# Performance work log

Measured on AMD Instinct MI355X. Metric: run time of the kernel, lower is better.

The kernel has to match this reference:

```python
import jax, jax.numpy as jnp
import numpy as np
from jax import lax

B, L, C, P = 512, 6, 4, 45

def _conv(x, w, b, pad):
    y = lax.conv_general_dilated(x, w, (1, 1), [(pad, pad), (pad, pad)],
                                 dimension_numbers=('NCHW', 'OIHW', 'NCHW'))
    return y + b[None, :, None, None]

def _maxpool2(x):
    return lax.reduce_window(x, -jnp.inf, lax.max, (1, 1, 2, 2), (1, 1, 2, 2), 'VALID')

def _prelu(x, a):
    return jnp.where(x >= 0, x, a * x)

def setup_inputs() -> dict:
    key = jax.random.key(0)
    ks = jax.random.split(key, 16)
    s = 0.05
    inp = {
        'x': jax.random.normal(ks[0], (B, L, C, P, P), jnp.float32),
        'w0': jax.random.normal(ks[1], (32, C, 5, 5), jnp.float32) * s,
        'b0': jnp.zeros((32,), jnp.float32),
        'w1': jax.random.normal(ks[2], (32, 32, 5, 5), jnp.float32) * s,
        'b1': jnp.zeros((32,), jnp.float32),
        'w2': jax.random.normal(ks[3], (64, 32, 4, 4), jnp.float32) * s,
        'b2': jnp.zeros((64,), jnp.float32),
        'w3': jax.random.normal(ks[4], (64, 64, 3, 3), jnp.float32) * s,
        'b3': jnp.zeros((64,), jnp.float32),
        'a0': jnp.float32(0.25), 'a1': jnp.float32(0.25),
        'a2': jnp.float32(0.25), 'a3': jnp.float32(0.25),
        'fc1_w': jax.random.normal(ks[5], (L, 256, 128), jnp.float32) * s,
        'fc1_b': jnp.zeros((L, 128), jnp.float32),
        'a4': jnp.full((L, 1), 0.25, jnp.float32),
        'fc2_w': jax.random.normal(ks[6], (L, 128, 64), jnp.float32) * s,
        'fc2_b': jnp.zeros((L, 64), jnp.float32),
        'a5': jnp.full((L, 1), 0.25, jnp.float32),
        'fc3_w': jax.random.normal(ks[7], (L, 64, 4), jnp.float32) * s,
        'fc3_b': jnp.zeros((L, 4), jnp.float32),
    }
    return inp

def reference(x, w0, b0, w1, b1, w2, b2, w3, b3, a0, a1, a2, a3,
              fc1_w, fc1_b, a4, fc2_w, fc2_b, a5, fc3_w, fc3_b):
    b, l = x.shape[0], x.shape[1]
    # Conv tower shares weights across landmarks -> fold landmark into batch.
    h = x.reshape(b * l, x.shape[2], P, P)
    h = _maxpool2(_prelu(_conv(h, w0, b0, 1), a0))   # (BL,32,21,21)
    h = _maxpool2(_prelu(_conv(h, w1, b1, 1), a1))   # (BL,32,9,9)
    h = _maxpool2(_prelu(_conv(h, w2, b2, 1), a2))   # (BL,64,4,4)
    h = _prelu(_conv(h, w3, b3, 0), a3)              # (BL,64,2,2)
    h = h.reshape(b, l, 256)
    # Per-landmark FC heads as batched GEMMs.
    h = _prelu(jnp.einsum('bli,lio->blo', h, fc1_w) + fc1_b, a4)
    h = _prelu(jnp.einsum('bli,lio->blo', h, fc2_w) + fc2_b, a5)
    out = jnp.einsum('bli,lio->blo', h, fc3_w) + fc3_b   # (B,L,4)
    return out
```

## Files before the change

### kernel.cpp

```cpp
#include <hip/hip_runtime.h>
#include <stdint.h>

typedef _Float16 f16;
typedef _Float16 half8 __attribute__((ext_vector_type(8)));
typedef _Float16 half4 __attribute__((ext_vector_type(4)));
typedef float floatx16 __attribute__((ext_vector_type(16)));

#define NIMG 3072

#define WS_W0T   0
#define WS_W1T   10240
#define WS_W2T   61440
#define WS_W3T   126976
#define WS_FC1T  200704
#define WS_FC2T  593920
#define WS_FC3T  692224
#define WS_H3F   16646144

#define Z16 {0.f,0.f,0.f,0.f,0.f,0.f,0.f,0.f,0.f,0.f,0.f,0.f,0.f,0.f,0.f,0.f}

#define TOF(t) ((((t) > 24 ? 24 : (t)) / 5) * 208 + (((t) > 24 ? 24 : (t)) % 5) * 4)

__global__ __launch_bounds__(256) void k_prep(
    const float* __restrict__ w0, const float* __restrict__ w1, const float* __restrict__ w2,
    const float* __restrict__ w3, const float* __restrict__ fc1w, const float* __restrict__ fc2w,
    const float* __restrict__ fc3w,
    f16* __restrict__ w0t, f16* __restrict__ w1t, f16* __restrict__ w2t, f16* __restrict__ w3t,
    f16* __restrict__ fc1t, f16* __restrict__ fc2t, f16* __restrict__ fc3t)
{
  int stride = gridDim.x * blockDim.x;
  int g0 = blockIdx.x * blockDim.x + threadIdx.x;
  for (int i = g0; i < 3584; i += stride) {
    int j = i & 7, co = (i >> 3) & 31, hf = (i >> 8) & 1, t = i >> 9;
    int k = t * 16 + hf * 8 + j, tap = k >> 2, ci = k & 3;
    f16 v = (f16)0.f;
    if (tap < 25) { int ky = tap / 5, kx = tap % 5; v = (f16)w0[((co * 4 + ci) * 5 + ky) * 5 + kx]; }
    w0t[i] = v;
  }
  for (int i = g0; i < 25600; i += stride) {
    int j = i & 7, co = (i >> 3) & 31, hf = (i >> 8) & 1, ch = (i >> 9) & 1, tap = i >> 10;
    int ci = ch * 16 + hf * 8 + j, ky = tap / 5, kx = tap % 5;
    w1t[i] = (f16)w1[((co * 32 + ci) * 5 + ky) * 5 + kx];
  }
  for (int i = g0; i < 32768; i += stride) {
    int j = i & 7, co = (i >> 3) & 31, hf = (i >> 8) & 1, ct = (i >> 9) & 1, ch = (i >> 10) & 1, tap = i >> 11;
    int ci = ch * 16 + hf * 8 + j, cog = ct * 32 + co, ky = tap >> 2, kx = tap & 3;
    w2t[i] = (f16)w2[((cog * 32 + ci) * 4 + ky) * 4 + kx];
  }
  for (int i = g0; i < 36864; i += stride) {
    int j = i & 7, col = (i >> 3) & 31, hf = (i >> 8) & 1, ct = (i >> 9) & 1, c = i >> 10;
    int k = c * 16 + hf * 8 + j, tap = k >> 6, ci = k & 63, co = ct * 32 + col;
    int ky = tap / 3, kx = tap % 3;
    w3t[i] = (f16)w3[((co * 64 + ci) * 3 + ky) * 3 + kx];
  }
  for (int i = g0; i < 196608; i += stride) {
    int j = i & 7, col = (i >> 3) & 31, hf = (i >> 8) & 1, nt = (i >> 9) & 3, c = (i >> 11) & 15, l = i >> 15;
    int k = c * 16 + hf * 8 + j, o = nt * 32 + col;
    fc1t[i] = (f16)fc1w[(l * 256 + k) * 128 + o];
  }
  for (int i = g0; i < 49152; i += stride) {
    int j = i & 7, col = (i >> 3) & 31, hf = (i >> 8) & 1, nt = (i >> 9) & 1, c = (i >> 10) & 7, l = i >> 13;
    int k = c * 16 + hf * 8 + j, o = nt * 32 + col;
    fc2t[i] = (f16)fc2w[(l * 128 + k) * 64 + o];
  }
  for (int i = g0; i < 12288; i += stride) {
    int j = i & 7, col = (i >> 3) & 31, hf = (i >> 8) & 1, c = (i >> 9) & 3, l = i >> 11;
    int k = c * 16 + hf * 8 + j;
    f16 v = (f16)0.f;
    if (col < 4) v = (f16)fc3w[(l * 64 + k) * 4 + col];
    fc3t[i] = v;
  }
}

__global__ __launch_bounds__(512, 6) void k_conv012(
    const float* __restrict__ x,
    const f16* __restrict__ w0t, const float* __restrict__ b0, const float* __restrict__ a0p,
    const f16* __restrict__ w1t, const float* __restrict__ b1, const float* __restrict__ a1p,
    const f16* __restrict__ w2t, const float* __restrict__ b2, const float* __restrict__ a2p,
    f16* __restrict__ h3f)
{
  __shared__ __align__(16) uint32_t smem_u[12688];
  f16* sh   = (f16*)smem_u;
  f16* s_h1 = sh;
  f16* s_x  = sh + 22880;

  const int n = blockIdx.x, tid = threadIdx.x;
  const int wv = tid >> 6, l = tid & 63;
  const int hf = l >> 5, m = l & 31, dr = m >> 3, dc = m & 7, col = m;
  const float a0 = a0p[0], a1 = a1p[0];
  const float b0c = b0[col], b1c = b1[col];
  const half8* w0t8 = (const half8*)w0t;
  const half8* w1t8 = (const half8*)w1t;
  const half8* w2t8 = (const half8*)w2t;

  for (int i = tid; i < 2096; i += 512) {
    int cell = i >> 4, wi = i & 15, r, c;
    if (cell < 26) { r = 0; c = cell; }
    else { int j = cell - 26; r = j / 5 + 1; int c5 = j % 5; c = (c5 == 0) ? 0 : 21 + c5; }
    smem_u[(r * 26 + c) * 20 + wi] = 0u;
  }

  half8 B0[7];
  #pragma unroll
  for (int q = 0; q < 7; ++q)
    B0[q] = w0t8[(q * 2 + hf) * 32 + col];

  const int cdr = (m & 1) | ((m & 8) >> 2);
  const int cdc = ((m >> 1) & 3) | ((m & 16) >> 2);
  const float* xin = x + n * 8100;

  for (int band = 0; band < 6; ++band) {
    const int lo    = (band < 5) ? band * 8 : 38;
    const int nrows = (band < 5) ? 12 : 8;
    const int tend  = (band < 5) ? band * 12 + 12 : 66;
    for (int i = tid; i < nrows * 52; i += 512) {
      int rp = lo + i / 52, cp = i % 52;
      half4 h = {(f16)0, (f16)0, (f16)0, (f16)0};
      if (rp >= 1 && rp <= 45 && cp >= 1 && cp <= 45) {
        const float* px = xin + (rp - 1) * 45 + (cp - 1);
        h[0] = (f16)px[0];
        h[1] = (f16)px[2025];
        h[2] = (f16)px[4050];
        h[3] = (f16)px[6075];
      }
      *(half4*)(s_x + ((rp - lo) * 52 + cp) * 4) = h;
    }
    __syncthreads();
    for (int t = band * 12 + wv; t < tend; t += 8) {
      int g = t / 6;
      int r0 = 4 * g; if (r0 > 38) r0 = 38;
      int cb = (t % 6) * 8;
      int rowb = r0 - lo + cdr, colb = cb + cdc;
      const f16* base = s_x + (rowb * 52 + colb) * 4;
      floatx16 acc = Z16;
      #pragma unroll
      for (int q = 0; q < 7; ++q) {
        const int offL = hf ? TOF(4 * q + 2) : TOF(4 * q);
        half4 lo4 = *(const half4*)(base + offL);
        half4 hi4;
        if (q < 6) {
          const int offH = hf ? TOF(4 * q + 3) : TOF(4 * q + 1);
          hi4 = *(const half4*)(base + offH);
        } else {
          hi4 = (half4){(f16)0, (f16)0, (f16)0, (f16)0};
        }
        half8 av = __builtin_shufflevector(lo4, hi4, 0, 1, 2, 3, 4, 5, 6, 7);
        acc = __builtin_amdgcn_mfma_f32_32x32x16_f16(av, B0[q], acc, 0, 0, 0);
      }
      #pragma unroll
      for (int q = 0; q < 4; ++q) {
        float v = fmaxf(fmaxf(acc[4*q], acc[4*q + 1]), fmaxf(acc[4*q + 2], acc[4*q + 3]));
        v += b0c; v = (v >= 0.f) ? v : a0 * v;
        int pr = (r0 >> 1) + (q & 1), pc = (cb >> 1) + hf + 2 * (q >> 1);
        if (pc < 21) s_h1[((pr + 1) * 26 + (pc + 1)) * 40 + col] = (f16)v;
      }
    }
    __syncthreads();
  }

  int t0 = wv * 2;
  int t1 = t0 + 1; if (t1 > 14) t1 = 14;
  int r0a = 4 * (t0 / 3); if (r0a > 14) r0a = 14;
  int cca = 8 * (t0 % 3); if (cca > 14) cca = 14;
  int r0b = 4 * (t1 / 3); if (r0b > 14) r0b = 14;
  int ccb = 8 * (t1 % 3); if (ccb > 14) ccb = 14;
  const f16* pAa = s_h1 + ((r0a + dr) * 26 + cca + dc) * 40 + hf * 8;
  const f16* pAb = s_h1 + ((r0b + dr) * 26 + ccb + dc) * 40 + hf * 8;
  floatx16 accA = Z16;
  floatx16 accB = Z16;
  for (int ky = 0; ky < 5; ++ky) {
    const half8* wb = w1t8 + ky * 640 + hf * 32 + col;
    const f16* qa = pAa + ky * 1040;
    const f16* qb = pAb + ky * 1040;
    #pragma unroll
    for (int kx = 0; kx < 5; ++kx) {
      #pragma unroll
      for (int ch = 0; ch < 2; ++ch) {
        half8 b  = wb[kx * 128 + ch * 64];
        half8 aA = *(const half8*)(qa + kx * 40 + ch * 16);
        half8 aB = *(const half8*)(qb + kx * 40 + ch * 16);
        accA = __builtin_amdgcn_mfma_f32_32x32x16_f16(aA, b, accA, 0, 0, 0);
        accB = __builtin_amdgcn_mfma_f32_32x32x16_f16(aB, b, accB, 0, 0, 0);
      }
    }
  }
  __syncthreads();

  f16* s2 = sh;
  for (int i = tid; i < 640; i += 512) {
    int cell = i >> 4, wi = i & 15, r, c;
    if (cell < 11)      { r = 0;  c = cell; }
    else if (cell < 22) { r = 10; c = cell - 11; }
    else if (cell < 31) { r = cell - 21; c = 0; }
    else                { r = cell - 30; c = 10; }
    smem_u[(r * 14 + c) * 20 + wi] = 0u;
  }
  #pragma unroll
  for (int tt = 0; tt < 2; ++tt) {
    const floatx16 acc = tt ? accB : accA;
    int r0 = tt ? r0b : r0a, cc = tt ? ccb : cca;
    #pragma unroll
    for (int pp = 0; pp < 2; ++pp)
      #pragma unroll
      for (int c2 = 0; c2 < 2; ++c2) {
        float v = fmaxf(fmaxf(acc[8*pp + 2*c2], acc[8*pp + 2*c2 + 1]),
                        fmaxf(acc[8*pp + 4 + 2*c2], acc[8*pp + 4 + 2*c2 + 1]));
        v += b1c; v = (v >= 0.f) ? v : a1 * v;
        int pr = (r0 >> 1) + pp, pc = (cc >> 1) + 2 * hf + c2;
        if (pc < 9) s2[((pr + 1) * 14 + (pc + 1)) * 40 + col] = (f16)v;
      }
  }
  __syncthreads();

  if (wv < 4) {
    const int mt = wv >> 1, c2t = wv & 1;
    const float a2 = a2p[0];
    const float b2c = b2[c2t * 32 + col];
    const f16* pA = s2 + ((mt * 4 + dr) * 14 + dc) * 40 + hf * 8;
    floatx16 acc = Z16;
    #pragma unroll 4
    for (int tap = 0; tap < 16; ++tap) {
      int aoff = ((tap >> 2) * 14 + (tap & 3)) * 40;
      #pragma unroll
      for (int ch = 0; ch < 2; ++ch) {
        half8 b = w2t8[tap * 256 + ch * 128 + c2t * 64 + hf * 32 + col];
        half8 a = *(const half8*)(pA + aoff + ch * 16);
        acc = __builtin_amdgcn_mfma_f32_32x32x16_f16(a, b, acc, 0, 0, 0);
      }
    }
    f16* o = h3f + n * 1024;
    #pragma unroll
    for (int pp = 0; pp < 2; ++pp)
      #pragma unroll
      for (int c2 = 0; c2 < 2; ++c2) {
        float v = fmaxf(fmaxf(acc[8*pp + 2*c2], acc[8*pp + 2*c2 + 1]),
                        fmaxf(acc[8*pp + 4 + 2*c2], acc[8*pp + 4 + 2*c2 + 1]));
        v += b2c; v = (v >= 0.f) ? v : a2 * v;
        int pr = mt * 2 + pp, pc = 2 * hf + c2;
        o[(pr * 4 + pc) * 64 + c2t * 32 + col] = (f16)v;
      }
  }
}

__global__ __launch_bounds__(256) void k_tail(
    const f16* __restrict__ h3f,
    const f16* __restrict__ w3t, const float* __restrict__ b3, const float* __restrict__ a3p,
    const f16* __restrict__ fc1t, const float* __restrict__ fc1b, const float* __restrict__ a4,
    const f16* __restrict__ fc2t, const float* __restrict__ fc2b, const float* __restrict__ a5,
    const f16* __restrict__ fc3t, const float* __restrict__ fc3b,
    float* __restrict__ out)
{
  __shared__ __align__(16) f16 s_feat[32 * 264];
  __shared__ __align__(16) f16 s_g1[32 * 136];
  __shared__ __align__(16) f16 s_g2[32 * 72];

  const int lm = blockIdx.x % 6, t = blockIdx.x / 6;
  const int tid = threadIdx.x, wv = tid >> 6, lane = tid & 63;
  const int hf = lane >> 5, col = lane & 31;
  const half8* w3t8  = (const half8*)w3t;
  const half8* fc1t8 = (const half8*)fc1t;
  const half8* fc2t8 = (const half8*)fc2t;
  const half8* fc3t8 = (const half8*)fc3t;

  {
    const int mt = wv;
    const int i_img = mt * 8 + (col >> 2);
    const int pos = col & 3, oy = pos >> 1, ox = pos & 1;
    const int gimg = (t * 32 + i_img) * 6 + lm;
    const f16* Abase = h3f + gimg * 1024 + (oy * 4 + ox) * 64;
    floatx16 acc0 = Z16, acc1 = Z16;
    for (int c = 0; c < 36; ++c) {
      int tap = c >> 2;
      int ky = tap / 3, kx = tap % 3;
      half8 a = *(const half8*)(Abase + (ky * 4 + kx) * 64 + (c & 3) * 16 + hf * 8);
      half8 bb0 = w3t8[((c * 2 + 0) * 2 + hf) * 32 + col];
      half8 bb1 = w3t8[((c * 2 + 1) * 2 + hf) * 32 + col];
      acc0 = __builtin_amdgcn_mfma_f32_32x32x16_f16(a, bb0, acc0, 0, 0, 0);
      acc1 = __builtin_amdgcn_mfma_f32_32x32x16_f16(a, bb1, acc1, 0, 0, 0);
    }
    const float a3 = a3p[0];
    #pragma unroll
    for (int ct = 0; ct < 2; ++ct) {
      const floatx16 acc = ct ? acc1 : acc0;
      const int co = ct * 32 + col;
      const float bb = b3[co];
      #pragma unroll
      for (int q = 0; q < 4; ++q) {
        int ii = mt * 8 + 2 * q + hf;
        half4 w;
        #pragma unroll
        for (int z = 0; z < 4; ++z) {
          float v = acc[q * 4 + z] + bb;
          v = (v >= 0.f) ? v : a3 * v;
          w[z] = (f16)v;
        }
        *(half4*)(s_feat + ii * 264 + co * 4) = w;
      }
    }
  }
  __syncthreads();

  {
    floatx16 g = Z16;
    for (int c = 0; c < 16; ++c) {
      half8 a = *(const half8*)(s_feat + col * 264 + c * 16 + hf * 8);
      half8 b = fc1t8[(((lm * 16 + c) * 4 + wv) * 2 + hf) * 32 + col];
      g = __builtin_amdgcn_mfma_f32_32x32x16_f16(a, b, g, 0, 0, 0);
    }
    const float a4v = a4[lm];
    const float bb = fc1b[lm * 128 + wv * 32 + col];
    #pragma unroll
    for (int reg = 0; reg < 16; ++reg) {
      int r = (reg & 3) + 8 * (reg >> 2) + 4 * hf;
      float v = g[reg] + bb;
      v = (v >= 0.f) ? v : a4v * v;
      s_g1[r * 136 + wv * 32 + col] = (f16)v;
    }
  }
  __syncthreads();

  if (wv < 2) {
    floatx16 g = Z16;
    for (int c = 0; c < 8; ++c) {
      half8 a = *(const half8*)(s_g1 + col * 136 + c * 16 + hf * 8);
      half8 b = fc2t8[(((lm * 8 + c) * 2 + wv) * 2 + hf) * 32 + col];
      g = __builtin_amdgcn_mfma_f32_32x32x16_f16(a, b, g, 0, 0, 0);
    }
    const float a5v = a5[lm];
    const float bb = fc2b[lm * 64 + wv * 32 + col];
    #pragma unroll
    for (int reg = 0; reg < 16; ++reg) {
      int r = (reg & 3) + 8 * (reg >> 2) + 4 * hf;
      float v = g[reg] + bb;
      v = (v >= 0.f) ? v : a5v * v;
      s_g2[r * 72 + wv * 32 + col] = (f16)v;
    }
  }
  __syncthreads();

  if (wv == 0) {
    floatx16 g = Z16;
    for (int c = 0; c < 4; ++c) {
      half8 a = *(const half8*)(s_g2 + col * 72 + c * 16 + hf * 8);
      half8 b = fc3t8[((lm * 4 + c) * 2 + hf) * 32 + col];
      g = __builtin_amdgcn_mfma_f32_32x32x16_f16(a, b, g, 0, 0, 0);
    }
    if (col < 4) {
      const float bb = fc3b[lm * 4 + col];
      #pragma unroll
      for (int reg = 0; reg < 16; ++reg) {
        int r = (reg & 3) + 8 * (reg >> 2) + 4 * hf;
        out[((t * 32 + r) * 6 + lm) * 4 + col] = g[reg] + bb;
      }
    }
  }
}

extern "C" void kernel_launch(void* const* d_in, const int* in_sizes, int n_in,
                              void* d_out, int out_size, void* d_ws, size_t ws_size,
                              hipStream_t stream) {
  const float* x    = (const float*)d_in[0];
  const float* w0   = (const float*)d_in[1];
  const float* b0   = (const float*)d_in[2];
  const float* w1   = (const float*)d_in[3];
  const float* b1   = (const float*)d_in[4];
  const float* w2   = (const float*)d_in[5];
  const float* b2   = (const float*)d_in[6];
  const float* w3   = (const float*)d_in[7];
  const float* b3   = (const float*)d_in[8];
  const float* a0   = (const float*)d_in[9];
  const float* a1   = (const float*)d_in[10];
  const float* a2   = (const float*)d_in[11];
  const float* a3   = (const float*)d_in[12];
  const float* fc1w = (const float*)d_in[13];
  const float* fc1b = (const float*)d_in[14];
  const float* a4   = (const float*)d_in[15];
  const float* fc2w = (const float*)d_in[16];
  const float* fc2b = (const float*)d_in[17];
  const float* a5   = (const float*)d_in[18];
  const float* fc3w = (const float*)d_in[19];
  const float* fc3b = (const float*)d_in[20];
  float* out = (float*)d_out;

  char* ws = (char*)d_ws;
  f16* w0t  = (f16*)(ws + WS_W0T);
  f16* w1t  = (f16*)(ws + WS_W1T);
  f16* w2t  = (f16*)(ws + WS_W2T);
  f16* w3t  = (f16*)(ws + WS_W3T);
  f16* fc1t = (f16*)(ws + WS_FC1T);
  f16* fc2t = (f16*)(ws + WS_FC2T);
  f16* fc3t = (f16*)(ws + WS_FC3T);
  f16* h3f  = (f16*)(ws + WS_H3F);

  k_prep   <<<128, 256, 0, stream>>>(w0, w1, w2, w3, fc1w, fc2w, fc3w,
                                     w0t, w1t, w2t, w3t, fc1t, fc2t, fc3t);
  k_conv012<<<NIMG, 512, 0, stream>>>(x, w0t, b0, a0, w1t, b1, a1, w2t, b2, a2, h3f);
  k_tail   <<<96, 256, 0, stream>>>(h3f, w3t, b3, a3, fc1t, fc1b, a4,
                                    fc2t, fc2b, a5, fc3t, fc3b, out);
}
```

Baseline: 335.5 us.

## Use larger conv0 row bands and serialize conv1 tiles to cut registers

Conv0 input staging now uses 4 bands of 16 rows instead of 6 bands of 12 rows. This cuts the number of staging passes and block barriers, at the cost of a slightly larger shared-memory buffer. Conv1 now computes its two tiles one after the other through a lambda, reducing each to a pooled half4 right away instead of holding two 16-float accumulators live. This should lower register pressure, but gives up the interleaved MFMA issue that shared the weight loads between the two tiles.

```diff
diff --git a/kernel.cpp b/kernel.cpp
--- a/kernel.cpp
+++ b/kernel.cpp
@@ -79,7 +79,7 @@
     const f16* __restrict__ w2t, const float* __restrict__ b2, const float* __restrict__ a2p,
     f16* __restrict__ h3f)
 {
-  __shared__ __align__(16) uint32_t smem_u[12688];
+  __shared__ __align__(16) uint32_t smem_u[13104];
   f16* sh   = (f16*)smem_u;
   f16* s_h1 = sh;
   f16* s_x  = sh + 22880;
@@ -109,10 +109,11 @@
   const int cdc = ((m >> 1) & 3) | ((m & 16) >> 2);
   const float* xin = x + n * 8100;
 
-  for (int band = 0; band < 6; ++band) {
-    const int lo    = (band < 5) ? band * 8 : 38;
-    const int nrows = (band < 5) ? 12 : 8;
-    const int tend  = (band < 5) ? band * 12 + 12 : 66;
+  for (int band = 0; band < 4; ++band) {
+    const int lo    = (band < 3) ? band * 12 : 36;
+    const int nrows = (band < 3) ? 16 : 10;
+    const int tst   = band * 18;
+    const int tend  = (band < 3) ? tst + 18 : 66;
     for (int i = tid; i < nrows * 52; i += 512) {
       int rp = lo + i / 52, cp = i % 52;
       half4 h = {(f16)0, (f16)0, (f16)0, (f16)0};
@@ -126,7 +127,7 @@
       *(half4*)(s_x + ((rp - lo) * 52 + cp) * 4) = h;
     }
     __syncthreads();
-    for (int t = band * 12 + wv; t < tend; t += 8) {
+    for (int t = tst + wv; t < tend; t += 8) {
       int g = t / 6;
       int r0 = 4 * g; if (r0 > 38) r0 = 38;
       int cb = (t % 6) * 8;
@@ -158,32 +159,40 @@
     __syncthreads();
   }
 
-  int t0 = wv * 2;
-  int t1 = t0 + 1; if (t1 > 14) t1 = 14;
-  int r0a = 4 * (t0 / 3); if (r0a > 14) r0a = 14;
-  int cca = 8 * (t0 % 3); if (cca > 14) cca = 14;
-  int r0b = 4 * (t1 / 3); if (r0b > 14) r0b = 14;
-  int ccb = 8 * (t1 % 3); if (ccb > 14) ccb = 14;
-  const f16* pAa = s_h1 + ((r0a + dr) * 26 + cca + dc) * 40 + hf * 8;
-  const f16* pAb = s_h1 + ((r0b + dr) * 26 + ccb + dc) * 40 + hf * 8;
-  floatx16 accA = Z16;
-  floatx16 accB = Z16;
-  for (int ky = 0; ky < 5; ++ky) {
-    const half8* wb = w1t8 + ky * 640 + hf * 32 + col;
-    const f16* qa = pAa + ky * 1040;
-    const f16* qb = pAb + ky * 1040;
-    #pragma unroll
-    for (int kx = 0; kx < 5; ++kx) {
-      #pragma unroll
-      for (int ch = 0; ch < 2; ++ch) {
-        half8 b  = wb[kx * 128 + ch * 64];
-        half8 aA = *(const half8*)(qa + kx * 40 + ch * 16);
-        half8 aB = *(const half8*)(qb + kx * 40 + ch * 16);
-        accA = __builtin_amdgcn_mfma_f32_32x32x16_f16(aA, b, accA, 0, 0, 0);
-        accB = __builtin_amdgcn_mfma_f32_32x32x16_f16(aB, b, accB, 0, 0, 0);
-      }
-    }
-  }
+  auto conv1_tile = [&](int tq) -> half4 {
+    int r0 = 4 * (tq / 3); if (r0 > 14) r0 = 14;
+    int cc = 8 * (tq % 3); if (cc > 14) cc = 14;
+    const f16* pA = s_h1 + ((r0 + dr) * 26 + cc + dc) * 40 + hf * 8;
+    floatx16 acc = Z16;
+    for (int ky = 0; ky < 5; ++ky) {
+      const half8* wb = w1t8 + ky * 640 + hf * 32 + col;
+      const f16* qa = pA + ky * 1040;
+      #pragma unroll
+      for (int kx = 0; kx < 5; ++kx) {
+        #pragma unroll
+        for (int ch = 0; ch < 2; ++ch) {
+          half8 b = wb[kx * 128 + ch * 64];
+          half8 a = *(const half8*)(qa + kx * 40 + ch * 16);
+          acc = __builtin_amdgcn_mfma_f32_32x32x16_f16(a, b, acc, 0, 0, 0);
+        }
+      }
+    }
+    half4 w;
+    #pragma unroll
+    for (int pp = 0; pp < 2; ++pp)
+      #pragma unroll
+      for (int c2 = 0; c2 < 2; ++c2) {
+        float v = fmaxf(fmaxf(acc[8*pp + 2*c2], acc[8*pp + 2*c2 + 1]),
+                        fmaxf(acc[8*pp + 4 + 2*c2], acc[8*pp + 4 + 2*c2 + 1]));
+        v += b1c; v = (v >= 0.f) ? v : a1 * v;
+        w[pp * 2 + c2] = (f16)v;
+      }
+    return w;
+  };
+  const int tq0 = wv * 2;
+  int tq1 = tq0 + 1; if (tq1 > 14) tq1 = 14;
+  half4 wr0 = conv1_tile(tq0);
+  half4 wr1 = conv1_tile(tq1);
   __syncthreads();
 
   f16* s2 = sh;
@@ -197,17 +206,16 @@
   }
   #pragma unroll
   for (int tt = 0; tt < 2; ++tt) {
-    const floatx16 acc = tt ? accB : accA;
-    int r0 = tt ? r0b : r0a, cc = tt ? ccb : cca;
+    const int tq = tt ? tq1 : tq0;
+    const half4 wr = tt ? wr1 : wr0;
+    int r0 = 4 * (tq / 3); if (r0 > 14) r0 = 14;
+    int cc = 8 * (tq % 3); if (cc > 14) cc = 14;
     #pragma unroll
     for (int pp = 0; pp < 2; ++pp)
       #pragma unroll
       for (int c2 = 0; c2 < 2; ++c2) {
-        float v = fmaxf(fmaxf(acc[8*pp + 2*c2], acc[8*pp + 2*c2 + 1]),
-                        fmaxf(acc[8*pp + 4 + 2*c2], acc[8*pp + 4 + 2*c2 + 1]));
-        v += b1c; v = (v >= 0.f) ? v : a1 * v;
         int pr = (r0 >> 1) + pp, pc = (cc >> 1) + 2 * hf + c2;
-        if (pc < 9) s2[((pr + 1) * 14 + (pc + 1)) * 40 + col] = (f16)v;
+        if (pc < 9) s2[((pr + 1) * 14 + (pc + 1)) * 40 + col] = wr[pp * 2 + c2];
       }
   }
   __syncthreads();
```

Measured after the change: 330.7 us. No clear change (-1.4%).
